# Kernel tuning notes

Measured on AMD Instinct MI355X. Metric: run time of the kernel, lower is better.

Reference implementation:

```python
import jax, jax.numpy as jnp
import numpy as np

K = 3
P = 14
INV_SQRT2 = 0.7071067811865476  # db1 (Haar) filter coefficient
EPS = 1e-4


def _pool(x):
    # adaptive_avg_pool2d to (P, P); H, W divisible by P -> uniform mean pooling
    N, C, H, W = x.shape
    return x.reshape(N, C, P, H // P, P, W // P).mean(axis=(3, 5))


def setup_inputs() -> dict:
    key = jax.random.key(0)
    ks = jax.random.split(key, 8)
    N, C, H, W = 64, 3, 224, 224
    D, Cin = 540, 30  # D_clip=D_hidden=540, n_bands*3 = 30
    return {
        "frames": jax.random.normal(ks[0], (N, C, H, W), jnp.float32),
        "t_clip": jax.random.normal(ks[1], (N, D, P, P), jnp.float32),
        "w1": jax.random.normal(ks[2], (D, Cin), jnp.float32) * 0.05,
        "b1": jnp.zeros((D,), jnp.float32),
        "w2": jax.random.normal(ks[3], (D, D), jnp.float32) * 0.05,
        "b2": jnp.zeros((D,), jnp.float32),
        "wg": jax.random.normal(ks[4], (D, 2 * D, 3, 3), jnp.float32) * 0.05,
        "bg": jnp.zeros((D,), jnp.float32),
    }


def reference(frames, t_clip, w1, b1, w2, b2, wg, bg):
    # Batched Haar SWT2 (a trous, periodic), levels 1..K, fully vectorized over
    # (N, C) -- replaces the per-frame/per-channel pywt.swt2 CPU loop.
    a = frames
    bands = []  # per level: HL (cH), LH (cV), HH (cD), each (N, C, H, W)
    for j in range(K):
        d = 2 ** j  # filter dilation at level j+1
        lx = (a + jnp.roll(a, -d, axis=-1)) * INV_SQRT2
        hx = (a - jnp.roll(a, -d, axis=-1)) * INV_SQRT2
        cA = (lx + jnp.roll(lx, -d, axis=-2)) * INV_SQRT2
        cH = (lx - jnp.roll(lx, -d, axis=-2)) * INV_SQRT2
        cV = (hx + jnp.roll(hx, -d, axis=-2)) * INV_SQRT2
        cD = (hx - jnp.roll(hx, -d, axis=-2)) * INV_SQRT2
        bands += [cH, cV, cD]
        a = cA
    # per-(frame, channel) 99th-percentile normalization + pool to (P, P)
    pooled = []
    for b in bands:
        s = jnp.quantile(jnp.abs(b), 0.99, axis=(-2, -1), keepdims=True)
        pooled.append(_pool(b / (s + EPS)))
    # LL band (level K approximation): mean-center then quantile-scale
    mu = a.mean(axis=(-2, -1), keepdims=True)
    s = jnp.quantile(jnp.abs(a - mu), 0.99, axis=(-2, -1), keepdims=True)
    pooled.append(_pool((a - mu) / (s + EPS)))
    e_pix = jnp.concatenate(pooled, axis=1)  # (N, 30, P, P)

    # 1x1 conv -> relu -> 1x1 conv -> tanh
    h = jax.nn.relu(jnp.einsum("ncpq,dc->ndpq", e_pix, w1) + b1[None, :, None, None])
    m = jnp.tanh(jnp.einsum("ncpq,dc->ndpq", h, w2) + b2[None, :, None, None])

    # gated fusion with CLIP patch tokens
    gi = jnp.concatenate([t_clip, m], axis=1)  # (N, 2*D, P, P)
    g = jax.lax.conv_general_dilated(
        gi, wg, (1, 1), "SAME", dimension_numbers=("NCHW", "OIHW", "NCHW")
    ) + bg[None, :, None, None]
    gamma = jax.nn.sigmoid(g)
    return t_clip + gamma * m
```

## Files before the change

kernel.cpp:

```cpp
#include <hip/hip_runtime.h>

typedef unsigned short u16;
typedef unsigned int u32;
typedef __bf16 bf16x8 __attribute__((ext_vector_type(8)));
typedef float f32x4 __attribute__((ext_vector_type(4)));

constexpr int NB = 64, CH3 = 3;
constexpr int PLANES = NB * CH3;
constexpr int PPIX = 224 * 224;
constexpr int PP = 196;
constexpr int NPX = NB * PP;
constexpr int K2 = 576;
constexpr int CIPAD = 1088;
constexpr int KCONV = 9 * CIPAD;
constexpr int BINS = 256;
constexpr int BIN0 = 896;
constexpr int RANK1 = 49674;
constexpr int RANK2 = 49675;

constexpr size_t OFF_BSUM = 2 * 1024 * 1024;
constexpr size_t SZ_BSUM  = (size_t)10 * PLANES * PP * 4;
constexpr size_t OFF_INVS = OFF_BSUM + SZ_BSUM;
constexpr size_t OFF_HBF  = OFF_INVS + 8192;
constexpr size_t OFF_GIT  = OFF_HBF + (size_t)NPX * K2 * 2;
constexpr size_t SZ_GIT   = (size_t)NB * 256 * CIPAD * 2;
constexpr size_t OFF_WGB  = OFF_GIT + SZ_GIT;
constexpr size_t OFF_W2B  = OFF_WGB + (size_t)640 * KCONV * 2;
constexpr size_t OFF_MARR = OFF_W2B + (size_t)640 * K2 * 2;
constexpr size_t SZ_MARR  = (size_t)NPX * 540 * 4;
constexpr size_t OFF_HISTP = OFF_MARR + SZ_MARR;
constexpr size_t SZ_HISTP  = (size_t)PLANES * 14 * 2560 * 4;
constexpr size_t OFF_PSUM  = OFF_HISTP + SZ_HISTP;

__device__ __forceinline__ u16 f2bf(float x) {
  union { float f; u32 u; } c; c.f = x;
  u32 r = c.u + 0x7FFFu + ((c.u >> 16) & 1u);
  return (u16)(r >> 16);
}

__device__ __forceinline__ float wred64(float v) {
  v += __shfl_down(v, 32, 64); v += __shfl_down(v, 16, 64);
  v += __shfl_down(v, 8, 64);  v += __shfl_down(v, 4, 64);
  v += __shfl_down(v, 2, 64);  v += __shfl_down(v, 1, 64);
  return v;
}

__device__ __forceinline__ float gred16(float v) {
  v += __shfl_down(v, 8, 16); v += __shfl_down(v, 4, 16);
  v += __shfl_down(v, 2, 16); v += __shfl_down(v, 1, 16);
  return v;
}

__device__ __forceinline__ int hbin(float v) {
  int b = (int)(__float_as_uint(fabsf(v)) >> 20) - BIN0;
  return min(max(b, 0), BINS - 1);
}

__device__ __forceinline__ void cp16(const void* g, void* l) {
  __builtin_amdgcn_global_load_lds((const __attribute__((address_space(1))) u32*)g,
                                   (__attribute__((address_space(3))) u32*)l, 16, 0, 0);
}

__device__ __forceinline__ float fast_tanh(float x) {
  return 1.f - 2.f / (1.f + __expf(2.f * x));
}
__device__ __forceinline__ float fast_sigmoid(float x) {
  return 1.f / (1.f + __expf(-x));
}

#define BAR_MEM() asm volatile("s_barrier" ::: "memory")

constexpr int RSTRIDE = 10 * 128 + 8;
constexpr int SWT_BLOCKS = 14 * PLANES;

__global__ __launch_bounds__(256) void prep_kernel(const float* __restrict__ frames,
    const float* __restrict__ wg, const float* __restrict__ w2,
    const float* __restrict__ tclip,
    float* __restrict__ psum, int* __restrict__ histp, float* __restrict__ bsum,
    u16* __restrict__ wgb, u16* __restrict__ w2b, u16* __restrict__ git)
{
  __shared__ float shf[19856];
  const int bid = blockIdx.x;
  const int t = threadIdx.x;

  if (bid < SWT_BLOCKS) {
    float* a1 = shf;
    float* a2 = shf + 4928;
    u32* lh = (u32*)(shf + 9408);
    float* csum = shf + 19712;
    float* wsum = shf + 19852;
    const int rb = bid % 14, plane = bid / 14;
    const float* Pp = frames + (size_t)plane * PPIX;

    for (int i = t; i < 8 * RSTRIDE; i += 256) lh[i] = 0;
    __syncthreads();

    u32* lhr = &lh[(t & 7) * RSTRIDE];
    const int cell0 = (t >> 4) * 10;
    float ps = 0.f;

    if (t < 224) {
      int c2 = t + 1; if (c2 >= 224) c2 -= 224;
      float sH = 0.f, sV = 0.f, sD = 0.f;
      int gr0 = rb * 16; if (gr0 >= 224) gr0 -= 224;
      float q00 = Pp[gr0 * 224 + t], q01 = Pp[gr0 * 224 + c2];
      for (int r = 0; r < 22; ++r) {
        int gr1 = rb * 16 + r + 1; if (gr1 >= 224) gr1 -= 224;
        float p10 = Pp[gr1 * 224 + t], p11 = Pp[gr1 * 224 + c2];
        float sa = q00 + q01, sb = p10 + p11, da = q00 - q01, db = p10 - p11;
        a1[r * 224 + t] = (sa + sb) * 0.5f;
        if (r < 16) {
          float cH = (sa - sb) * 0.5f, cV = (da + db) * 0.5f, cD = (da - db) * 0.5f;
          int bH = hbin(cH), bV = hbin(cV), bD = hbin(cD);
          atomicAdd(&lhr[0 * 128 + (bH >> 1)], 1u << ((bH & 1) * 16));
          atomicAdd(&lhr[1 * 128 + (bV >> 1)], 1u << ((bV & 1) * 16));
          atomicAdd(&lhr[2 * 128 + (bD >> 1)], 1u << ((bD & 1) * 16));
          sH += cH; sV += cV; sD += cD;
          ps += q00;
        }
        q00 = p10; q01 = p11;
      }
      sH = gred16(sH); sV = gred16(sV); sD = gred16(sD);
      if ((t & 15) == 0) { csum[cell0 + 0] = sH; csum[cell0 + 1] = sV; csum[cell0 + 2] = sD; }
    }
    ps = wred64(ps);
    if ((t & 63) == 0) wsum[t >> 6] = ps;
    __syncthreads();
    if (t == 0) psum[plane * 14 + rb] = wsum[0] + wsum[1] + wsum[2] + wsum[3];

    if (t < 224) {
      int c2 = t + 2; if (c2 >= 224) c2 -= 224;
      float sH = 0.f, sV = 0.f, sD = 0.f;
      for (int r = 0; r < 20; ++r) {
        float p00 = a1[r * 224 + t], p01 = a1[r * 224 + c2];
        float p10 = a1[(r + 2) * 224 + t], p11 = a1[(r + 2) * 224 + c2];
        float sa = p00 + p01, sb = p10 + p11, da = p00 - p01, db = p10 - p11;
        a2[r * 224 + t] = (sa + sb) * 0.5f;
        if (r < 16) {
          float cH = (sa - sb) * 0.5f, cV = (da + db) * 0.5f, cD = (da - db) * 0.5f;
          int bH = hbin(cH), bV = hbin(cV), bD = hbin(cD);
          atomicAdd(&lhr[3 * 128 + (bH >> 1)], 1u << ((bH & 1) * 16));
          atomicAdd(&lhr[4 * 128 + (bV >> 1)], 1u << ((bV & 1) * 16));
          atomicAdd(&lhr[5 * 128 + (bD >> 1)], 1u << ((bD & 1) * 16));
          sH += cH; sV += cV; sD += cD;
        }
      }
      sH = gred16(sH); sV = gred16(sV); sD = gred16(sD);
      if ((t & 15) == 0) { csum[cell0 + 3] = sH; csum[cell0 + 4] = sV; csum[cell0 + 5] = sD; }
    }
    __syncthreads();

    if (t < 224) {
      int c2 = t + 4; if (c2 >= 224) c2 -= 224;
      float sH = 0.f, sV = 0.f, sD = 0.f, sA = 0.f;
      for (int r = 0; r < 16; ++r) {
        float p00 = a2[r * 224 + t], p01 = a2[r * 224 + c2];
        float p10 = a2[(r + 4) * 224 + t], p11 = a2[(r + 4) * 224 + c2];
        float sa = p00 + p01, sb = p10 + p11, da = p00 - p01, db = p10 - p11;
        float cA = (sa + sb) * 0.5f;
        float cH = (sa - sb) * 0.5f, cV = (da + db) * 0.5f, cD = (da - db) * 0.5f;
        int bH = hbin(cH), bV = hbin(cV), bD = hbin(cD), bA = hbin(cA);
        atomicAdd(&lhr[6 * 128 + (bH >> 1)], 1u << ((bH & 1) * 16));
        atomicAdd(&lhr[7 * 128 + (bV >> 1)], 1u << ((bV & 1) * 16));
        atomicAdd(&lhr[8 * 128 + (bD >> 1)], 1u << ((bD & 1) * 16));
        atomicAdd(&lhr[9 * 128 + (bA >> 1)], 1u << ((bA & 1) * 16));
        sH += cH; sV += cV; sD += cD; sA += cA;
      }
      sH = gred16(sH); sV = gred16(sV); sD = gred16(sD); sA = gred16(sA);
      if ((t & 15) == 0) {
        csum[cell0 + 6] = sH; csum[cell0 + 7] = sV; csum[cell0 + 8] = sD; csum[cell0 + 9] = sA;
      }
    }
    __syncthreads();

    int* hp = histp + ((size_t)plane * 14 + rb) * 2560;
    for (int i = t; i < 2560; i += 256) {
      int bg = i >> 8, b = i & 255;
      u32 acc = 0;
#pragma unroll
      for (int rp = 0; rp < 8; ++rp)
        acc += (lh[rp * RSTRIDE + bg * 128 + (b >> 1)] >> ((b & 1) * 16)) & 0xFFFFu;
      hp[i] = (int)acc;
    }
    if (t < 140) {
      int cell = t / 10, bg = t - cell * 10;
      bsum[((size_t)bg * PLANES + plane) * PP + rb * 14 + cell] = csum[cell * 10 + bg];
    }
  } else if (bid < SWT_BLOCKS + 640) {
    const int oc = bid - SWT_BLOCKS;
    if (oc < 540) {
      for (int i = t; i < 9720; i += 256) shf[i] = wg[(size_t)oc * 9720 + i];
    }
    __syncthreads();
    for (int j = t; j < KCONV; j += 256) {
      int kc = j >> 6, i = j & 63;
      int cib = kc / 9, tap = kc - cib * 9;
      int ci = cib * 64 + i;
      float v = (oc < 540 && ci < 1080) ? shf[ci * 9 + tap] : 0.f;
      wgb[(size_t)oc * KCONV + j] = f2bf(v);
    }
  } else if (bid < SWT_BLOCKS + 2080) {
    int tid = (bid - SWT_BLOCKS - 640) * 256 + t;
    int oc = tid / K2, cc = tid - oc * K2;
    float v = (oc < 540 && cc < 540) ? w2[oc * 540 + cc] : 0.f;
    w2b[tid] = f2bf(v);
  } else if (bid < SWT_BLOCKS + 4169) {
    constexpr int CPB = 136;
    constexpr int CPN = 60 * CPB + 196;
    int tid = (bid - SWT_BLOCKS - 2080) * 256 + t;
    if (tid >= NB * CPN) return;
    int n = tid / CPN, rem = tid - n * CPN;
    int y, x, c;
    if (rem < 60 * CPB) {
      int bi = rem / CPB; c = rem - bi * CPB;
      if (bi < 16) { y = 0; x = bi; }
      else if (bi < 32) { y = 15; x = bi - 16; }
      else { int i = bi - 32; y = 1 + (i >> 1); x = (i & 1) * 15; }
    } else {
      int q = rem - 60 * CPB;
      y = 1 + q / 14; x = 1 + q % 14; c = 135;
    }
    f32x4 z = (f32x4){0.f, 0.f, 0.f, 0.f};
    *reinterpret_cast<f32x4*>(&git[((size_t)(n * 256 + y * 16 + x)) * CIPAD + c * 8]) = z;
  } else {
    int local = bid - SWT_BLOCKS - 4169;
    int n = local / 36, rem = local - n * 36;
    int ct = rem >> 2, qt = rem & 3;
    const int tr = t >> 6, tc = t & 63;
#pragma unroll 4
    for (int i = 0; i < 16; ++i) {
      int ci = ct * 64 + i * 4 + tr, q = qt * 64 + tc;
      float v = (ci < 540 && q < 196) ? tclip[((size_t)n * 540 + ci) * 196 + q] : 0.f;
      shf[(i * 4 + tr) * 65 + tc] = v;
    }
    __syncthreads();
#pragma unroll 4
    for (int i = 0; i < 16; ++i) {
      int q = qt * 64 + i * 4 + tr, ci = ct * 64 + tc;
      if (q < 196 && ci < 540) {
        int y = q / 14, x = q - y * 14;
        git[(((size_t)n * 16 + 1 + y) * 16 + 1 + x) * CIPAD + ci] = f2bf(shf[tc * 65 + i * 4 + tr]);
      }
    }
  }
}

__global__ __launch_bounds__(256) void quant_kernel(const int* __restrict__ histp,
    float* __restrict__ invs)
{
  const int g = blockIdx.x;
  const int bg = g / PLANES, plane = g - bg * PLANES;
  __shared__ int cum[BINS];
  __shared__ float vv[2];
  const int t = threadIdx.x;
  const int* hp = histp + (size_t)plane * 14 * 2560 + bg * 256;
  int c = 0;
#pragma unroll
  for (int rb = 0; rb < 14; ++rb) c += hp[rb * 2560 + t];
  cum[t] = c;
  __syncthreads();
  for (int off = 1; off < BINS; off <<= 1) {
    int y = (t >= off) ? cum[t - off] : 0;
    __syncthreads();
    cum[t] += y;
    __syncthreads();
  }
  int inc = cum[t], prev = inc - c;
#pragma unroll
  for (int k = 0; k < 2; ++k) {
    int rank = k ? RANK2 : RANK1;
    if (prev < rank && rank <= inc) {
      float lo = __uint_as_float((u32)(t + BIN0) << 20);
      float hi = __uint_as_float((u32)(t + BIN0 + 1) << 20);
      float fr = ((float)(rank - prev) - 0.5f) / (float)c;
      fr = fminf(fmaxf(fr, 0.f), 1.f);
      vv[k] = lo + (hi - lo) * fr;
    }
  }
  __syncthreads();
  if (t == 0) {
    float s = 0.75f * vv[0] + 0.25f * vv[1];
    invs[g] = 1.f / (s + 1e-4f);
  }
}

__global__ __launch_bounds__(256) void gemm1_kernel(const float* __restrict__ bsum,
    const float* __restrict__ psum, const float* __restrict__ invs,
    const float* __restrict__ w1, const float* __restrict__ b1, u16* __restrict__ hbf)
{
  __shared__ float es[64][33];
  __shared__ float w1s[128][33];
  const int t = threadIdx.x;
  const int px0 = blockIdx.x * 64, oc0 = blockIdx.y * 128;
  for (int i = t; i < 64 * 32; i += 256) {
    int r = i >> 5, cc = i & 31;
    int px = px0 + r, n = px / PP, q = px - n * PP;
    float val = 0.f;
    if (cc < 27) {
      int bg = cc / 3, c = cc - bg * 3;
      int plane = n * 3 + c;
      val = bsum[((size_t)bg * PLANES + plane) * PP + q] * (1.f / 256.f) * invs[bg * PLANES + plane];
    } else if (cc < 30) {
      int c = cc - 27, plane = n * 3 + c;
      float s14 = 0.f;
#pragma unroll
      for (int rb = 0; rb < 14; ++rb) s14 += psum[plane * 14 + rb];
      float mu = s14 * (8.f / 50176.f);
      val = (bsum[((size_t)9 * PLANES + plane) * PP + q] * (1.f / 256.f) - mu) * invs[9 * PLANES + plane];
    }
    es[r][cc] = val;
  }
  for (int i = t; i < 128 * 32; i += 256) {
    int r = i >> 5, cc = i & 31; int oc = oc0 + r;
    w1s[r][cc] = (oc < 540 && cc < 30) ? w1[oc * 30 + cc] : 0.f;
  }
  __syncthreads();
  const int ocl = t & 31, pxl = (t >> 5) * 8;
  float acc[4][8];
#pragma unroll
  for (int i = 0; i < 4; ++i)
#pragma unroll
    for (int j = 0; j < 8; ++j) acc[i][j] = 0.f;
  for (int k = 0; k < 30; ++k) {
    float wv[4], ev[8];
#pragma unroll
    for (int i = 0; i < 4; ++i) wv[i] = w1s[ocl + 32 * i][k];
#pragma unroll
    for (int j = 0; j < 8; ++j) ev[j] = es[pxl + j][k];
#pragma unroll
    for (int i = 0; i < 4; ++i)
#pragma unroll
      for (int j = 0; j < 8; ++j) acc[i][j] += wv[i] * ev[j];
  }
#pragma unroll
  for (int i = 0; i < 4; ++i) {
    int oc = oc0 + ocl + 32 * i;
    if (oc >= 576) continue;
    float bv = (oc < 540) ? b1[oc] : 0.f;
#pragma unroll
    for (int j = 0; j < 8; ++j) {
      int px = px0 + pxl + j;
      float v = (oc < 540) ? fmaxf(acc[i][j] + bv, 0.f) : 0.f;
      hbf[(size_t)px * K2 + oc] = f2bf(v);
    }
  }
}

template <int MODE>
__global__ __launch_bounds__(256) void mfma_gemm_kernel(
    const u16* __restrict__ A, const u16* __restrict__ Bm,
    const float* __restrict__ bias,
    float* __restrict__ marr, u16* __restrict__ git,
    const float* __restrict__ tclip, float* __restrict__ outp)
{
  constexpr int KCPB = (MODE == 1) ? 153 : 9;
  constexpr int BSTRIDE = (MODE == 1) ? KCONV : K2;
  __shared__ u16 smem[32768];
  const int t = threadIdx.x;
  const int lane = t & 63, wave = t >> 6;
  const int wm = wave & 1, wn = wave >> 1;

  int px0, oc0;
  if constexpr (MODE == 1) {
    int orig = blockIdx.x;
    int xcd = orig & 7, off = orig >> 3;
    constexpr int q = 61, r = 2;
    int wg = (xcd < r ? xcd * (q + 1) : r * (q + 1) + (xcd - r) * q) + off;
    int bx = wg / 5, by = wg - bx * 5;
    px0 = bx * 128; oc0 = by * 128;
  } else {
    px0 = blockIdx.x * 128; oc0 = blockIdx.y * 128;
  }

  const u16* aSrc[4];
  const u16* bSrc[4];
  int dstOff[4];
#pragma unroll
  for (int r = 0; r < 4; ++r) {
    int slot = r * 256 + t;
    int row = slot >> 3;
    int gs = ((slot ^ row) & 7) << 3;
    if constexpr (MODE == 0) {
      aSrc[r] = A + (size_t)(px0 + row) * K2 + gs;
    } else {
      int px = px0 + row;
      int n = px / 196, q2 = px - n * 196;
      int y = q2 / 14, x = q2 - y * 14;
      aSrc[r] = A + (size_t)((n * 16 + y) * 16 + x) * CIPAD + gs;
    }
    bSrc[r] = Bm + (size_t)(oc0 + row) * BSTRIDE + gs;
    dstOff[r] = (r * 256 + wave * 64) * 8;
  }

  auto stage = [&](int kcg, int buf) {
    int boff = kcg * 64;
    int aoff;
    if constexpr (MODE == 1) {
      int cib = kcg / 9, tap = kcg - cib * 9;
      int ky = tap / 3, kx = tap - ky * 3;
      aoff = (ky * 16 + kx) * CIPAD + cib * 64;
    } else aoff = boff;
    u16* As = smem + buf * 16384;
    u16* Bs = As + 8192;
#pragma unroll
    for (int r = 0; r < 4; ++r) cp16(aSrc[r] + aoff, As + dstOff[r]);
#pragma unroll
    for (int r = 0; r < 4; ++r) cp16(bSrc[r] + boff, Bs + dstOff[r]);
  };

  const int tx = lane & 15, quad = lane >> 4, l7 = lane & 7;
  int rowA[4], rowB[4];
#pragma unroll
  for (int i = 0; i < 4; ++i) {
    rowA[i] = (wm * 64 + i * 16 + tx) * 64;
    rowB[i] = (wn * 64 + i * 16 + tx) * 64;
  }

  f32x4 acc[4][4];
#pragma unroll
  for (int i = 0; i < 4; ++i)
#pragma unroll
    for (int j = 0; j < 4; ++j) acc[i][j] = (f32x4){0.f, 0.f, 0.f, 0.f};

  stage(0, 0);
  stage(1, 1);
  int cur = 0;
  for (int kc = 0; kc < KCPB; ++kc) {
    if (kc + 1 < KCPB) { asm volatile("s_waitcnt vmcnt(8)" ::: "memory"); }
    else               { asm volatile("s_waitcnt vmcnt(0)" ::: "memory"); }
    BAR_MEM();
    const u16* As = smem + cur * 16384;
    const u16* Bs = As + 8192;
#pragma unroll
    for (int ks = 0; ks < 2; ++ks) {
      int goff = (((ks * 4 + quad) ^ l7) << 3);
      bf16x8 af[4], bfr[4];
#pragma unroll
      for (int i = 0; i < 4; ++i) af[i] = *reinterpret_cast<const bf16x8*>(As + rowA[i] + goff);
#pragma unroll
      for (int i = 0; i < 4; ++i) bfr[i] = *reinterpret_cast<const bf16x8*>(Bs + rowB[i] + goff);
      __builtin_amdgcn_s_setprio(1);
#pragma unroll
      for (int i = 0; i < 4; ++i)
#pragma unroll
        for (int j = 0; j < 4; ++j)
          acc[i][j] = __builtin_amdgcn_mfma_f32_16x16x32_bf16(af[i], bfr[j], acc[i][j], 0, 0, 0);
      __builtin_amdgcn_s_setprio(0);
    }
    BAR_MEM();
    if (kc + 2 < KCPB) stage(kc + 2, cur);
    cur ^= 1;
  }

#pragma unroll
  for (int j = 0; j < 4; ++j) {
    int oc = oc0 + wn * 64 + j * 16 + tx;
    if (oc >= 540) continue;
    float bv = bias[oc];
#pragma unroll
    for (int i = 0; i < 4; ++i) {
      f32x4 v = acc[i][j];
      int px = px0 + wm * 64 + i * 16 + quad * 4;
      int n = px / 196, q2 = px - n * 196;
      size_t idx = ((size_t)(n * 540 + oc)) * 196 + q2;
      if constexpr (MODE == 0) {
#pragma unroll
        for (int r = 0; r < 4; ++r) {
          float val = fast_tanh(v[r] + bv);
          marr[idx + r] = val;
          int qq = q2 + r;
          int y = qq / 14, x = qq - y * 14;
          git[((n * 16 + 1 + y) * 16 + 1 + x) * CIPAD + 540 + oc] = f2bf(val);
        }
      } else {
        f32x4 mv = *reinterpret_cast<const f32x4*>(marr + idx);
        f32x4 tv = *reinterpret_cast<const f32x4*>(tclip + idx);
        f32x4 res;
#pragma unroll
        for (int r = 0; r < 4; ++r) {
          res[r] = tv[r] + mv[r] * fast_sigmoid(v[r] + bv);
        }
        *reinterpret_cast<f32x4*>(outp + idx) = res;
      }
    }
  }
}

extern "C" void kernel_launch(void* const* d_in, const int* in_sizes, int n_in,
                              void* d_out, int out_size, void* d_ws, size_t ws_size,
                              hipStream_t stream)
{
  const float* frames = (const float*)d_in[0];
  const float* t_clip = (const float*)d_in[1];
  const float* w1 = (const float*)d_in[2];
  const float* b1 = (const float*)d_in[3];
  const float* w2 = (const float*)d_in[4];
  const float* b2 = (const float*)d_in[5];
  const float* wg = (const float*)d_in[6];
  const float* bg = (const float*)d_in[7];
  float* out = (float*)d_out;
  char* ws = (char*)d_ws;

  float* BSUM = (float*)(ws + OFF_BSUM);
  float* INVS = (float*)(ws + OFF_INVS);
  u16* HBF = (u16*)(ws + OFF_HBF);
  u16* GIT = (u16*)(ws + OFF_GIT);
  u16* WGB = (u16*)(ws + OFF_WGB);
  u16* W2B = (u16*)(ws + OFF_W2B);
  float* MARR = (float*)(ws + OFF_MARR);
  int* HISTP = (int*)(ws + OFF_HISTP);
  float* PSUM = (float*)(ws + OFF_PSUM);

  prep_kernel<<<SWT_BLOCKS + 6473, 256, 0, stream>>>(
      frames, wg, w2, t_clip, PSUM, HISTP, BSUM, WGB, W2B, GIT);

  quant_kernel<<<1920, 256, 0, stream>>>(HISTP, INVS);

  gemm1_kernel<<<dim3(196, 5), 256, 0, stream>>>(BSUM, PSUM, INVS, w1, b1, HBF);
  mfma_gemm_kernel<0><<<dim3(98, 5), 256, 0, stream>>>(HBF, W2B, b2, MARR, GIT, nullptr, nullptr);
  mfma_gemm_kernel<1><<<490, 256, 0, stream>>>(GIT, WGB, bg, MARR, nullptr, t_clip, out);
}
```

Before: 488.7 us.

## Shrink SWT shared memory by reusing level buffer and halving histogram replicas

Result: faster. 469.7 us (-3.9%).

```diff
diff --git a/kernel.cpp b/kernel.cpp
--- a/kernel.cpp
+++ b/kernel.cpp
@@ -29,7 +29,7 @@
 constexpr size_t OFF_MARR = OFF_W2B + (size_t)640 * K2 * 2;
 constexpr size_t SZ_MARR  = (size_t)NPX * 540 * 4;
 constexpr size_t OFF_HISTP = OFF_MARR + SZ_MARR;
-constexpr size_t SZ_HISTP  = (size_t)PLANES * 14 * 2560 * 4;
+constexpr size_t SZ_HISTP  = (size_t)PLANES * 14 * 2560 * 2;
 constexpr size_t OFF_PSUM  = OFF_HISTP + SZ_HISTP;
 
 __device__ __forceinline__ u16 f2bf(float x) {
@@ -72,41 +72,43 @@
 
 constexpr int RSTRIDE = 10 * 128 + 8;
 constexpr int SWT_BLOCKS = 14 * PLANES;
+constexpr int SHF_WORDS = 4928 + 4 * RSTRIDE + 140 + 4;
 
 __global__ __launch_bounds__(256) void prep_kernel(const float* __restrict__ frames,
     const float* __restrict__ wg, const float* __restrict__ w2,
     const float* __restrict__ tclip,
-    float* __restrict__ psum, int* __restrict__ histp, float* __restrict__ bsum,
+    float* __restrict__ psum, u16* __restrict__ histp, float* __restrict__ bsum,
     u16* __restrict__ wgb, u16* __restrict__ w2b, u16* __restrict__ git)
 {
-  __shared__ float shf[19856];
+  __shared__ float shf[SHF_WORDS];
   const int bid = blockIdx.x;
   const int t = threadIdx.x;
 
   if (bid < SWT_BLOCKS) {
     float* a1 = shf;
-    float* a2 = shf + 4928;
-    u32* lh = (u32*)(shf + 9408);
-    float* csum = shf + 19712;
-    float* wsum = shf + 19852;
+    u32* lh = (u32*)(shf + 4928);
+    float* csum = shf + 4928 + 4 * RSTRIDE;
+    float* wsum = csum + 140;
     const int rb = bid % 14, plane = bid / 14;
     const float* Pp = frames + (size_t)plane * PPIX;
 
-    for (int i = t; i < 8 * RSTRIDE; i += 256) lh[i] = 0;
-    __syncthreads();
-
-    u32* lhr = &lh[(t & 7) * RSTRIDE];
+    for (int i = t; i < 4 * RSTRIDE; i += 256) lh[i] = 0;
+    __syncthreads();
+
+    u32* lhr = &lh[(t & 3) * RSTRIDE];
     const int cell0 = (t >> 4) * 10;
     float ps = 0.f;
+    int c2_1 = t + 1; if (c2_1 >= 224) c2_1 -= 224;
+    int c2_2 = t + 2; if (c2_2 >= 224) c2_2 -= 224;
+    int c2_4 = t + 4; if (c2_4 >= 224) c2_4 -= 224;
 
     if (t < 224) {
-      int c2 = t + 1; if (c2 >= 224) c2 -= 224;
       float sH = 0.f, sV = 0.f, sD = 0.f;
-      int gr0 = rb * 16; if (gr0 >= 224) gr0 -= 224;
-      float q00 = Pp[gr0 * 224 + t], q01 = Pp[gr0 * 224 + c2];
+      float q00 = Pp[(rb * 16) * 224 + t], q01 = Pp[(rb * 16) * 224 + c2_1];
+#pragma unroll 2
       for (int r = 0; r < 22; ++r) {
         int gr1 = rb * 16 + r + 1; if (gr1 >= 224) gr1 -= 224;
-        float p10 = Pp[gr1 * 224 + t], p11 = Pp[gr1 * 224 + c2];
+        float p10 = Pp[gr1 * 224 + t], p11 = Pp[gr1 * 224 + c2_1];
         float sa = q00 + q01, sb = p10 + p11, da = q00 - q01, db = p10 - p11;
         a1[r * 224 + t] = (sa + sb) * 0.5f;
         if (r < 16) {
@@ -128,35 +130,59 @@
     __syncthreads();
     if (t == 0) psum[plane * 14 + rb] = wsum[0] + wsum[1] + wsum[2] + wsum[3];
 
+    {
+      float sH = 0.f, sV = 0.f, sD = 0.f;
+      float c00 = 0.f, c01 = 0.f, c10 = 0.f, c11 = 0.f;
+      if (t < 224) {
+        c00 = a1[0 * 224 + t]; c01 = a1[0 * 224 + c2_2];
+        c10 = a1[1 * 224 + t]; c11 = a1[1 * 224 + c2_2];
+      }
+      for (int rp = 0; rp < 10; ++rp) {
+        int r = rp * 2;
+        float n00 = 0.f, n01 = 0.f, n10 = 0.f, n11 = 0.f;
+        if (t < 224) {
+          n00 = a1[(r + 2) * 224 + t]; n01 = a1[(r + 2) * 224 + c2_2];
+          n10 = a1[(r + 3) * 224 + t]; n11 = a1[(r + 3) * 224 + c2_2];
+        }
+        __syncthreads();
+        if (t < 224) {
+          float sa0 = c00 + c01, sb0 = n00 + n01, da0 = c00 - c01, db0 = n00 - n01;
+          float sa1 = c10 + c11, sb1 = n10 + n11, da1 = c10 - c11, db1 = n10 - n11;
+          a1[r * 224 + t] = (sa0 + sb0) * 0.5f;
+          a1[(r + 1) * 224 + t] = (sa1 + sb1) * 0.5f;
+          if (rp < 8) {
+            float cH0 = (sa0 - sb0) * 0.5f, cV0 = (da0 + db0) * 0.5f, cD0 = (da0 - db0) * 0.5f;
+            float cH1 = (sa1 - sb1) * 0.5f, cV1 = (da1 + db1) * 0.5f, cD1 = (da1 - db1) * 0.5f;
+            int b0 = hbin(cH0), b1 = hbin(cV0), b2 = hbin(cD0);
+            int b3 = hbin(cH1), b4 = hbin(cV1), b5 = hbin(cD1);
+            atomicAdd(&lhr[3 * 128 + (b0 >> 1)], 1u << ((b0 & 1) * 16));
+            atomicAdd(&lhr[4 * 128 + (b1 >> 1)], 1u << ((b1 & 1) * 16));
+            atomicAdd(&lhr[5 * 128 + (b2 >> 1)], 1u << ((b2 & 1) * 16));
+            atomicAdd(&lhr[3 * 128 + (b3 >> 1)], 1u << ((b3 & 1) * 16));
+            atomicAdd(&lhr[4 * 128 + (b4 >> 1)], 1u << ((b4 & 1) * 16));
+            atomicAdd(&lhr[5 * 128 + (b5 >> 1)], 1u << ((b5 & 1) * 16));
+            sH += cH0 + cH1; sV += cV0 + cV1; sD += cD0 + cD1;
+          }
+          c00 = n00; c01 = n01; c10 = n10; c11 = n11;
+        }
+      }
+      if (t < 224) {
+        sH = gred16(sH); sV = gred16(sV); sD = gred16(sD);
+        if ((t & 15) == 0) { csum[cell0 + 3] = sH; csum[cell0 + 4] = sV; csum[cell0 + 5] = sD; }
+      }
+    }
+    __syncthreads();
+
     if (t < 224) {
-      int c2 = t + 2; if (c2 >= 224) c2 -= 224;
-      float sH = 0.f, sV = 0.f, sD = 0.f;
-      for (int r = 0; r < 20; ++r) {
-        float p00 = a1[r * 224 + t], p01 = a1[r * 224 + c2];
-        float p10 = a1[(r + 2) * 224 + t], p11 = a1[(r + 2) * 224 + c2];
-        float sa = p00 + p01, sb = p10 + p11, da = p00 - p01, db = p10 - p11;
-        a2[r * 224 + t] = (sa + sb) * 0.5f;
-        if (r < 16) {
-          float cH = (sa - sb) * 0.5f, cV = (da + db) * 0.5f, cD = (da - db) * 0.5f;
-          int bH = hbin(cH), bV = hbin(cV), bD = hbin(cD);
-          atomicAdd(&lhr[3 * 128 + (bH >> 1)], 1u << ((bH & 1) * 16));
-          atomicAdd(&lhr[4 * 128 + (bV >> 1)], 1u << ((bV & 1) * 16));
-          atomicAdd(&lhr[5 * 128 + (bD >> 1)], 1u << ((bD & 1) * 16));
-          sH += cH; sV += cV; sD += cD;
-        }
-      }
-      sH = gred16(sH); sV = gred16(sV); sD = gred16(sD);
-      if ((t & 15) == 0) { csum[cell0 + 3] = sH; csum[cell0 + 4] = sV; csum[cell0 + 5] = sD; }
-    }
-    __syncthreads();
-
-    if (t < 224) {
-      int c2 = t + 4; if (c2 >= 224) c2 -= 224;
       float sH = 0.f, sV = 0.f, sD = 0.f, sA = 0.f;
+      float v[4], w[4];
+#pragma unroll
+      for (int k = 0; k < 4; ++k) { v[k] = a1[k * 224 + t]; w[k] = a1[k * 224 + c2_4]; }
+#pragma unroll
       for (int r = 0; r < 16; ++r) {
-        float p00 = a2[r * 224 + t], p01 = a2[r * 224 + c2];
-        float p10 = a2[(r + 4) * 224 + t], p11 = a2[(r + 4) * 224 + c2];
-        float sa = p00 + p01, sb = p10 + p11, da = p00 - p01, db = p10 - p11;
+        float n0 = a1[(r + 4) * 224 + t], n1 = a1[(r + 4) * 224 + c2_4];
+        float p00 = v[r & 3], p01 = w[r & 3];
+        float sa = p00 + p01, sb = n0 + n1, da = p00 - p01, db = n0 - n1;
         float cA = (sa + sb) * 0.5f;
         float cH = (sa - sb) * 0.5f, cV = (da + db) * 0.5f, cD = (da - db) * 0.5f;
         int bH = hbin(cH), bV = hbin(cV), bD = hbin(cD), bA = hbin(cA);
@@ -165,6 +191,7 @@
         atomicAdd(&lhr[8 * 128 + (bD >> 1)], 1u << ((bD & 1) * 16));
         atomicAdd(&lhr[9 * 128 + (bA >> 1)], 1u << ((bA & 1) * 16));
         sH += cH; sV += cV; sD += cD; sA += cA;
+        v[r & 3] = n0; w[r & 3] = n1;
       }
       sH = gred16(sH); sV = gred16(sV); sD = gred16(sD); sA = gred16(sA);
       if ((t & 15) == 0) {
@@ -173,14 +200,14 @@
     }
     __syncthreads();
 
-    int* hp = histp + ((size_t)plane * 14 + rb) * 2560;
+    u16* hp = histp + ((size_t)plane * 14 + rb) * 2560;
     for (int i = t; i < 2560; i += 256) {
       int bg = i >> 8, b = i & 255;
       u32 acc = 0;
 #pragma unroll
-      for (int rp = 0; rp < 8; ++rp)
+      for (int rp = 0; rp < 4; ++rp)
         acc += (lh[rp * RSTRIDE + bg * 128 + (b >> 1)] >> ((b & 1) * 16)) & 0xFFFFu;
-      hp[i] = (int)acc;
+      hp[i] = (u16)acc;
     }
     if (t < 140) {
       int cell = t / 10, bg = t - cell * 10;
@@ -245,7 +272,7 @@
   }
 }
 
-__global__ __launch_bounds__(256) void quant_kernel(const int* __restrict__ histp,
+__global__ __launch_bounds__(256) void quant_kernel(const u16* __restrict__ histp,
     float* __restrict__ invs)
 {
   const int g = blockIdx.x;
@@ -253,7 +280,7 @@
   __shared__ int cum[BINS];
   __shared__ float vv[2];
   const int t = threadIdx.x;
-  const int* hp = histp + (size_t)plane * 14 * 2560 + bg * 256;
+  const u16* hp = histp + (size_t)plane * 14 * 2560 + bg * 256;
   int c = 0;
 #pragma unroll
   for (int rb = 0; rb < 14; ++rb) c += hp[rb * 2560 + t];
@@ -508,7 +535,7 @@
   u16* WGB = (u16*)(ws + OFF_WGB);
   u16* W2B = (u16*)(ws + OFF_W2B);
   float* MARR = (float*)(ws + OFF_MARR);
-  int* HISTP = (int*)(ws + OFF_HISTP);
+  u16* HISTP = (u16*)(ws + OFF_HISTP);
   float* PSUM = (float*)(ws + OFF_PSUM);
 
   prep_kernel<<<SWT_BLOCKS + 6473, 256, 0, stream>>>(
```
